# Performance work log

Hardware: AMD Instinct MI355X
Metric: run time of the kernel (lower is better)

The kernel has to match this reference:

```python
import jax, jax.numpy as jnp
import numpy as np

B, T, D, H, C = 8, 1024, 1024, 16, 8  # batch, seq, d_model, heads, num_concepts
DK = D // H
LAMBD = 5.0


def setup_inputs() -> dict:
    key = jax.random.key(0)
    ks = jax.random.split(key, 14)
    s = 0.02
    return {
        "qa_concept": jax.random.normal(ks[0], (B, T, T, C), jnp.float32),
        "query": jax.random.normal(ks[1], (B, T, D), jnp.float32),
        "key": jax.random.normal(ks[2], (B, T, D), jnp.float32),
        "value": jax.random.normal(ks[3], (B, T, D), jnp.float32),
        "Wq": jax.random.normal(ks[4], (D, D), jnp.float32) * s,
        "bq": jnp.zeros((D,), jnp.float32),
        "Wk": jax.random.normal(ks[5], (D, D), jnp.float32) * s,
        "bk": jnp.zeros((D,), jnp.float32),
        "Wv": jax.random.normal(ks[6], (D, D), jnp.float32) * s,
        "bv": jnp.zeros((D,), jnp.float32),
        "Wo": jax.random.normal(ks[7], (D, D), jnp.float32) * s,
        "bo": jnp.zeros((D,), jnp.float32),
        "mask": jax.random.randint(ks[8], (B, T), 0, 2, jnp.int32),
    }


def reference(qa_concept, query, key, value, Wq, bq, Wk, bk, Wv, bv, Wo, bo, mask):
    # Linear projections (torch Linear: y = x @ W.T + b)
    q = (query @ Wq.T + bq).reshape(B, T, H, DK).transpose(0, 2, 1, 3)  # [B,H,T,dk]
    k = (key @ Wk.T + bk).reshape(B, T, H, DK).transpose(0, 2, 1, 3)
    v = (value @ Wv.T + bv).reshape(B, T, H, DK).transpose(0, 2, 1, 3)
    scores = jnp.einsum("bhqd,bhkd->bhqk", q, k) / jnp.sqrt(jnp.float32(DK))
    # concept bias added to first C heads only
    bias = LAMBD * jnp.transpose(qa_concept, (0, 3, 1, 2))  # [B,C,T,T]
    scores = scores.at[:, :C, :, :].add(bias)
    # mask: [B,T] -> [B,1,1,T], fill -1e9 where 0
    scores = jnp.where(mask[:, None, None, :] == 0, jnp.float32(-1e9), scores)
    attn = jax.nn.softmax(scores, axis=-1)  # dropout is identity in eval
    x = jnp.einsum("bhqk,bhkd->bhqd", attn, v)
    x = x.transpose(0, 2, 1, 3).reshape(B, T, D)
    return x @ Wo.T + bo
```

## Files before the change

### kernel.cpp

```cpp
#include <hip/hip_runtime.h>

#define B_  8
#define T_  1024
#define D_  1024
#define H_  16
#define DK_ 64
#define C_  8
#define N_  (B_*T_)

typedef __attribute__((ext_vector_type(8))) short bf16x8;
typedef __attribute__((ext_vector_type(4))) float f32x4;
typedef __attribute__((ext_vector_type(8))) unsigned short u16x8;
typedef __attribute__((ext_vector_type(4))) unsigned short u16x4;

__device__ __forceinline__ float bf2f(unsigned short u) {
  union { unsigned int i; float f; } x; x.i = ((unsigned int)u) << 16; return x.f;
}
__device__ __forceinline__ unsigned short f2bf(float f) {
  union { float f; unsigned int i; } x; x.f = f;
  unsigned int r = (x.i + 0x7fffu + ((x.i >> 16) & 1u)) >> 16;
  return (unsigned short)r;
}
__device__ __forceinline__ unsigned short f2h(float f) {
  union { _Float16 h; unsigned short u; } x; x.h = (_Float16)f; return x.u;
}
__device__ __forceinline__ float h2f(unsigned short u) {
  union { _Float16 h; unsigned short u; } x; x.u = u; return (float)x.h;
}

__device__ __forceinline__ void gl_lds16(const unsigned short* g, unsigned short* l) {
  __builtin_amdgcn_global_load_lds(
      (const __attribute__((address_space(1))) unsigned int*)g,
      (__attribute__((address_space(3))) unsigned int*)l,
      16, 0, 0);
}

__global__ __launch_bounds__(256) void cvt_qkv(
    const float* __restrict__ q, const float* __restrict__ k,
    const float* __restrict__ v, unsigned short* __restrict__ qo,
    unsigned short* __restrict__ ko, unsigned short* __restrict__ vo, int n4) {
  int seg = blockIdx.x >> 10;
  int bid = blockIdx.x & 1023;
  const float* in = (seg == 0) ? q : (seg == 1) ? k : v;
  unsigned short* out = (seg == 0) ? qo : (seg == 1) ? ko : vo;
  int tid = bid * blockDim.x + threadIdx.x;
  int stride = 1024 * 256;
  const float4* in4 = (const float4*)in;
  u16x4* out4 = (u16x4*)out;
  for (int i = tid; i < n4; i += stride) {
    float4 vv = in4[i];
    u16x4 o = { f2bf(vv.x), f2bf(vv.y), f2bf(vv.z), f2bf(vv.w) };
    out4[i] = o;
  }
}

__global__ __launch_bounds__(256) void cvt_w(
    const float* __restrict__ w0, const float* __restrict__ w1,
    const float* __restrict__ w2, const float* __restrict__ w3,
    unsigned short* __restrict__ o0, unsigned short* __restrict__ o1,
    unsigned short* __restrict__ o2, unsigned short* __restrict__ o3, int n4) {
  int seg = blockIdx.x >> 8;
  int bid = blockIdx.x & 255;
  const float* in = (seg == 0) ? w0 : (seg == 1) ? w1 : (seg == 2) ? w2 : w3;
  unsigned short* out = (seg == 0) ? o0 : (seg == 1) ? o1 : (seg == 2) ? o2 : o3;
  int tid = bid * blockDim.x + threadIdx.x;
  int stride = 256 * 256;
  const float4* in4 = (const float4*)in;
  u16x4* out4 = (u16x4*)out;
  for (int i = tid; i < n4; i += stride) {
    float4 vv = in4[i];
    u16x4 o = { f2bf(vv.x), f2bf(vv.y), f2bf(vv.z), f2bf(vv.w) };
    out4[i] = o;
  }
}

__global__ __launch_bounds__(256) void transposeQa(
    const float* __restrict__ qa, unsigned short* __restrict__ qat) {
  int b = blockIdx.x >> 10, q = blockIdx.x & 1023;
  int t = threadIdx.x;
  __shared__ float L[8][132];
  const float* src = qa + ((size_t)(b*T_ + q))*T_*C_;
  for (int ch = 0; ch < 8; ++ch) {
    int k0 = ch*128;
    float4 v = *(const float4*)(src + (size_t)(k0 + (t>>1))*C_ + (t&1)*4);
    int c4 = (t&1)*4, kk = t>>1;
    L[c4+0][kk] = v.x; L[c4+1][kk] = v.y; L[c4+2][kk] = v.z; L[c4+3][kk] = v.w;
    __syncthreads();
    int c = t >> 5, kk2 = (t&31)*4;
    float4 p = *(const float4*)&L[c][kk2];
    u16x4 o = { f2h(p.x), f2h(p.y), f2h(p.z), f2h(p.w) };
    *(u16x4*)(qat + ((size_t)(b*C_ + c)*T_ + q)*T_ + k0 + kk2) = o;
    __syncthreads();
  }
}

__global__ __launch_bounds__(256) void transposeV(
    const unsigned short* __restrict__ V, unsigned short* __restrict__ Vt) {
  int bid = blockIdx.x;
  int tt = bid & 15;
  int bh = bid >> 4;
  int b = bh >> 4, h = bh & 15;
  __shared__ unsigned short L[64][72];
  int r  = threadIdx.x >> 3;
  int c8 = (threadIdx.x & 7) * 8;
  const unsigned short* src = V + ((size_t)(b*T_ + tt*64))*D_ + h*64;
#pragma unroll
  for (int p = 0; p < 2; ++p) {
    int rr = r + p*32;
    u16x8 v = *(const u16x8*)(src + (size_t)rr*D_ + c8);
    *(u16x8*)&L[rr][c8] = v;
  }
  __syncthreads();
  unsigned short* dst = Vt + ((size_t)bh*64)*T_ + tt*64;
#pragma unroll
  for (int p = 0; p < 2; ++p) {
    int d = r + p*32;
    u16x8 o;
#pragma unroll
    for (int i = 0; i < 8; ++i) o[i] = L[c8 + i][d];
    *(u16x8*)(dst + (size_t)d*T_ + c8) = o;
  }
}

template <bool OUT_F32>
__device__ __forceinline__ void gemm_body(
    int blockid, const unsigned short* __restrict__ X,
    const unsigned short* __restrict__ W, const float* __restrict__ bias,
    void* __restrict__ Yv, unsigned short* As, unsigned short* Bs) {
  int orig = (blockid & 7) * 64 + (blockid >> 3);
  int bm = orig >> 3, bn = orig & 7;
  int t = threadIdx.x, lane = t & 63, w = t >> 6;
  int wr = w >> 1, wc = w & 1;
  int r16 = lane & 15, kg = lane >> 4;

  int srow0 = lane >> 2;
  int scol  = (lane & 3) * 8;
  const unsigned short* Ab = X + (size_t)(bm*128)*D_ + scol;
  const unsigned short* Bb = W + (size_t)(bn*128)*D_ + scol;

  f32x4 acc[4][4];
#pragma unroll
  for (int m = 0; m < 4; ++m)
#pragma unroll
    for (int n = 0; n < 4; ++n) acc[m][n] = (f32x4){0.f,0.f,0.f,0.f};

  for (int k0 = 0; k0 < D_; k0 += 32) {
    __syncthreads();
#pragma unroll
    for (int c = 0; c < 2; ++c) {
      int cidx = w*2 + c;
      int row = cidx*16 + srow0;
      gl_lds16(Ab + (size_t)row*D_ + k0, As + cidx*512);
      gl_lds16(Bb + (size_t)row*D_ + k0, Bs + cidx*512);
    }
    __syncthreads();

    bf16x8 a[4], bb[4];
#pragma unroll
    for (int m = 0; m < 4; ++m)
      a[m] = *(const bf16x8*)(As + (wr*64 + m*16 + r16)*32 + kg*8);
#pragma unroll
    for (int n = 0; n < 4; ++n)
      bb[n] = *(const bf16x8*)(Bs + (wc*64 + n*16 + r16)*32 + kg*8);
#pragma unroll
    for (int m = 0; m < 4; ++m)
#pragma unroll
      for (int n = 0; n < 4; ++n)
        acc[m][n] = __builtin_amdgcn_mfma_f32_16x16x32_bf16(a[m], bb[n], acc[m][n], 0, 0, 0);
  }

#pragma unroll
  for (int n = 0; n < 4; ++n) {
    int col = bn*128 + wc*64 + n*16 + r16;
    float bv = bias[col];
#pragma unroll
    for (int m = 0; m < 4; ++m) {
      int row0 = bm*128 + wr*64 + m*16 + kg*4;
#pragma unroll
      for (int jj = 0; jj < 4; ++jj) {
        float rv = acc[m][n][jj] + bv;
        if constexpr (OUT_F32)
          ((float*)Yv)[(size_t)(row0 + jj)*D_ + col] = rv;
        else
          ((unsigned short*)Yv)[(size_t)(row0 + jj)*D_ + col] = f2bf(rv);
      }
    }
  }
}

template <bool OUT_F32>
__global__ __launch_bounds__(256) void gemm_lds(
    const unsigned short* __restrict__ X, const unsigned short* __restrict__ W,
    const float* __restrict__ bias, void* __restrict__ Yv) {
  __shared__ __align__(16) unsigned short As[128*32];
  __shared__ __align__(16) unsigned short Bs[128*32];
  gemm_body<OUT_F32>(blockIdx.x, X, W, bias, Yv, As, Bs);
}

__global__ __launch_bounds__(256) void gemm_qkv(
    const unsigned short* __restrict__ Xq, const unsigned short* __restrict__ Xk,
    const unsigned short* __restrict__ Xv,
    const unsigned short* __restrict__ Wq2, const unsigned short* __restrict__ Wk2,
    const unsigned short* __restrict__ Wv2,
    const float* __restrict__ bq2, const float* __restrict__ bk2,
    const float* __restrict__ bv2,
    unsigned short* __restrict__ Yq, unsigned short* __restrict__ Yk,
    unsigned short* __restrict__ Yv2) {
  __shared__ __align__(16) unsigned short As[128*32];
  __shared__ __align__(16) unsigned short Bs[128*32];
  int seg = blockIdx.x >> 9, inner = blockIdx.x & 511;
  const unsigned short* X = (seg == 0) ? Xq : (seg == 1) ? Xk : Xv;
  const unsigned short* W = (seg == 0) ? Wq2 : (seg == 1) ? Wk2 : Wv2;
  const float* bias = (seg == 0) ? bq2 : (seg == 1) ? bk2 : bv2;
  unsigned short* Y = (seg == 0) ? Yq : (seg == 1) ? Yk : Yv2;
  gemm_body<false>(inner, X, W, bias, Y, As, Bs);
}

__global__ __launch_bounds__(256, 3) void attn4b(
    const unsigned short* __restrict__ Q, const unsigned short* __restrict__ K,
    const unsigned short* __restrict__ Vt, const unsigned short* __restrict__ qat,
    const int* __restrict__ mask, unsigned short* __restrict__ X) {
  int swzid = ((blockIdx.x & 7) << 7) | (blockIdx.x >> 3);
  int qt = swzid & 7, h = (swzid >> 3) & 15, b = swzid >> 7;
  int w = threadIdx.x >> 6, lane = threadIdx.x & 63;
  int r16 = lane & 15, kg = lane >> 4;
  int q0w = qt*128 + w*32;
  int bh = b*H_ + h;

  __shared__ unsigned short Ks[2][64][64];
  __shared__ unsigned short Vs[2][64][64];
  __shared__ unsigned int  P32[4][2][16][32];

  int rl = lane >> 3;
  int eo = ((lane & 7) * 8) ^ (rl << 3);
  const unsigned short* Kb = K + ((size_t)b*T_)*D_ + h*DK_;
  const unsigned short* Vb = Vt + ((size_t)bh*DK_)*T_;

  int sw16 = (r16 & 7) << 4;
  int ko0 = ((kg*16 +  0) ^ sw16) >> 1;
  int ko1 = ((kg*16 + 64) ^ sw16) >> 1;
  int sw32 = (r16 & 7) << 2;

  bf16x8 qfr[2][2];
#pragma unroll
  for (int qf = 0; qf < 2; ++qf) {
    const unsigned short* qrow = Q + ((size_t)b*T_ + q0w + qf*16 + r16)*D_ + h*DK_ + kg*8;
    qfr[qf][0] = *(const bf16x8*)qrow;
    qfr[qf][1] = *(const bf16x8*)(qrow + 32);
  }

  f32x4 acc[2][4];
#pragma unroll
  for (int qf = 0; qf < 2; ++qf)
#pragma unroll
    for (int db = 0; db < 4; ++db) acc[qf][db] = (f32x4){0.f,0.f,0.f,0.f};
  float mold[2] = {-3e38f, -3e38f};
  float lpart[2] = {0.f, 0.f};

  const int* mrow = mask + b*T_;
  const unsigned short* qab0 = qat + ((size_t)((b*C_ + h)*T_) + q0w + r16)*T_;

#pragma unroll
  for (int c = 0; c < 2; ++c) {
    int cc = w*2 + c;
    gl_lds16(Kb + (size_t)(cc*8 + rl)*D_ + eo, &Ks[0][cc*8][0]);
    gl_lds16(Vb + (size_t)(cc*8 + rl)*T_ + eo, &Vs[0][cc*8][0]);
  }
  __syncthreads();

  for (int t = 0; t < 16; ++t) {
    int k0 = t*64, bb = t & 1;
    if (t < 15) {
      int kn = k0 + 64, nb = bb ^ 1;
#pragma unroll
      for (int c = 0; c < 2; ++c) {
        int cc = w*2 + c;
        gl_lds16(Kb + (size_t)(kn + cc*8 + rl)*D_ + eo, &Ks[nb][cc*8][0]);
        gl_lds16(Vb + (size_t)(cc*8 + rl)*T_ + kn + eo, &Vs[nb][cc*8][0]);
      }
    }
    u16x4 qv[2][4];
    if (h < C_) {
#pragma unroll
      for (int qf = 0; qf < 2; ++qf)
#pragma unroll
        for (int kt = 0; kt < 4; ++kt)
          qv[qf][kt] = *(const u16x4*)(qab0 + (size_t)qf*16*T_ + k0 + kt*16 + kg*4);
    }
    int mk = mrow[k0 + lane];
    unsigned long long bits = __ballot(mk != 0);

    f32x4 s[2][4];
#pragma unroll
    for (int kt = 0; kt < 4; ++kt) {
      bf16x8 kf0 = *(const bf16x8*)&Ks[bb][kt*16 + r16][ko0];
      bf16x8 kf1 = *(const bf16x8*)&Ks[bb][kt*16 + r16][ko1];
#pragma unroll
      for (int qf = 0; qf < 2; ++qf) {
        f32x4 z = (f32x4){0.f,0.f,0.f,0.f};
        z = __builtin_amdgcn_mfma_f32_16x16x32_bf16(kf0, qfr[qf][0], z, 0, 0, 0);
        z = __builtin_amdgcn_mfma_f32_16x16x32_bf16(kf1, qfr[qf][1], z, 0, 0, 0);
        s[qf][kt] = z;
      }
    }

    float pmaxq[2];
#pragma unroll
    for (int qf = 0; qf < 2; ++qf) {
      float pmax = -3e38f;
#pragma unroll
      for (int kt = 0; kt < 4; ++kt)
#pragma unroll
        for (int jj = 0; jj < 4; ++jj) {
          float v = s[qf][kt][jj] * 0.125f;
          if (h < C_) v += 5.0f * h2f(qv[qf][kt][jj]);
          int idx = kt*16 + kg*4 + jj;
          v = ((bits >> idx) & 1ULL) ? v : -1e9f;
          s[qf][kt][jj] = v;
          pmax = fmaxf(pmax, v);
        }
      pmax = fmaxf(pmax, __shfl_xor(pmax, 16, 64));
      pmax = fmaxf(pmax, __shfl_xor(pmax, 32, 64));
      pmaxq[qf] = pmax;
    }
    if (!__all(pmaxq[0] - mold[0] <= 8.0f && pmaxq[1] - mold[1] <= 8.0f)) {
#pragma unroll
      for (int qf = 0; qf < 2; ++qf) {
        float mnew = fmaxf(mold[qf], pmaxq[qf]);
        float sc = __expf(mold[qf] - mnew);
        mold[qf] = mnew;
        lpart[qf] *= sc;
        float scq[4];
#pragma unroll
        for (int jj = 0; jj < 4; ++jj) scq[jj] = __shfl(sc, kg*4 + jj, 64);
#pragma unroll
        for (int db = 0; db < 4; ++db)
#pragma unroll
          for (int jj = 0; jj < 4; ++jj) acc[qf][db][jj] *= scq[jj];
      }
    }
#pragma unroll
    for (int qf = 0; qf < 2; ++qf) {
      unsigned int pk[8];
#pragma unroll
      for (int kt = 0; kt < 4; ++kt) {
        float p0 = __expf(s[qf][kt][0] - mold[qf]), p1 = __expf(s[qf][kt][1] - mold[qf]);
        float p2 = __expf(s[qf][kt][2] - mold[qf]), p3 = __expf(s[qf][kt][3] - mold[qf]);
        lpart[qf] += (p0 + p1) + (p2 + p3);
        pk[kt*2+0] = (unsigned)f2bf(p0) | ((unsigned)f2bf(p1) << 16);
        pk[kt*2+1] = (unsigned)f2bf(p2) | ((unsigned)f2bf(p3) << 16);
      }
#pragma unroll
      for (int kt = 0; kt < 4; ++kt)
        *(uint2*)&P32[w][qf][r16][(kt*8 + kg*2) ^ sw32] =
            make_uint2(pk[kt*2], pk[kt*2+1]);
    }
    __builtin_amdgcn_sched_barrier(0);
    asm volatile("s_waitcnt lgkmcnt(0)");
    __builtin_amdgcn_sched_barrier(0);
#pragma unroll
    for (int qf = 0; qf < 2; ++qf) {
      bf16x8 pa0 = *(const bf16x8*)&P32[w][qf][r16][(kg*4) ^ sw32];
      bf16x8 pa1 = *(const bf16x8*)&P32[w][qf][r16][(16 + kg*4) ^ sw32];
#pragma unroll
      for (int db = 0; db < 4; ++db) {
        bf16x8 vf0 = *(const bf16x8*)&Vs[bb][db*16 + r16][ko0];
        bf16x8 vf1 = *(const bf16x8*)&Vs[bb][db*16 + r16][ko1];
        acc[qf][db] = __builtin_amdgcn_mfma_f32_16x16x32_bf16(pa0, vf0, acc[qf][db], 0, 0, 0);
        acc[qf][db] = __builtin_amdgcn_mfma_f32_16x16x32_bf16(pa1, vf1, acc[qf][db], 0, 0, 0);
      }
    }
    __syncthreads();
  }

#pragma unroll
  for (int qf = 0; qf < 2; ++qf) {
    float lp = lpart[qf];
    lp += __shfl_xor(lp, 16, 64);
    lp += __shfl_xor(lp, 32, 64);
    float linv = 1.0f / lp;
    float invq[4];
#pragma unroll
    for (int jj = 0; jj < 4; ++jj) invq[jj] = __shfl(linv, kg*4 + jj, 64);
#pragma unroll
    for (int jj = 0; jj < 4; ++jj)
#pragma unroll
      for (int db = 0; db < 4; ++db)
        X[((size_t)b*T_ + q0w + qf*16 + kg*4 + jj)*D_ + h*DK_ + db*16 + r16] =
            f2bf(acc[qf][db][jj] * invq[jj]);
  }
}

__global__ __launch_bounds__(256) void attn_fused(
    const unsigned short* __restrict__ Q, const unsigned short* __restrict__ K,
    const unsigned short* __restrict__ Vt, const float* __restrict__ qa,
    const int* __restrict__ mask, unsigned short* __restrict__ X) {
  int bid = blockIdx.x;
  int qt = bid & 15, h = (bid >> 4) & 15, b = bid >> 8;
  int w = threadIdx.x >> 6, lane = threadIdx.x & 63;
  int r16 = lane & 15, kg = lane >> 4;
  int q0 = qt*64 + w*16;
  int bh = b*H_ + h;

  __shared__ unsigned short P[4][16][72];

  const unsigned short* qrow = Q + ((size_t)b*T_ + q0 + r16)*D_ + h*DK_ + kg*8;
  bf16x8 qf0 = *(const bf16x8*)qrow;
  bf16x8 qf1 = *(const bf16x8*)(qrow + 32);

  f32x4 acc[4];
#pragma unroll
  for (int db = 0; db < 4; ++db) acc[db] = (f32x4){0.f,0.f,0.f,0.f};
  float mrow[4], lrow[4];
#pragma unroll
  for (int jj = 0; jj < 4; ++jj) { mrow[jj] = -3e38f; lrow[jj] = 0.f; }

  const int* mptr = mask + b*T_;
  const unsigned short* Kbase = K + ((size_t)b*T_)*D_ + h*DK_;
  const unsigned short* Vbase = Vt + ((size_t)bh*DK_)*T_;
  const float* qabase = qa + ((size_t)(b*T_ + q0 + kg*4))*T_*C_ + h;

  for (int k0 = 0; k0 < T_; k0 += 64) {
    f32x4 s[4];
#pragma unroll
    for (int kt = 0; kt < 4; ++kt) {
      const unsigned short* krow = Kbase + (size_t)(k0 + kt*16 + r16)*D_ + kg*8;
      f32x4 z = (f32x4){0.f,0.f,0.f,0.f};
      z = __builtin_amdgcn_mfma_f32_16x16x32_bf16(qf0, *(const bf16x8*)krow,        z, 0, 0, 0);
      z = __builtin_amdgcn_mfma_f32_16x16x32_bf16(qf1, *(const bf16x8*)(krow + 32), z, 0, 0, 0);
      s[kt] = z;
    }
    int mk[4];
#pragma unroll
    for (int kt = 0; kt < 4; ++kt) mk[kt] = mptr[k0 + kt*16 + r16];
    if (h < C_) {
#pragma unroll
      for (int kt = 0; kt < 4; ++kt)
#pragma unroll
        for (int jj = 0; jj < 4; ++jj) {
          float bb = qabase[(size_t)jj*T_*C_ + (size_t)(k0 + kt*16 + r16)*C_];
          s[kt][jj] = s[kt][jj]*0.125f + 5.0f*bb;
        }
    } else {
#pragma unroll
      for (int kt = 0; kt < 4; ++kt)
#pragma unroll
        for (int jj = 0; jj < 4; ++jj) s[kt][jj] *= 0.125f;
    }
#pragma unroll
    for (int kt = 0; kt < 4; ++kt)
#pragma unroll
      for (int jj = 0; jj < 4; ++jj)
        if (mk[kt] == 0) s[kt][jj] = -1e9f;

#pragma unroll
    for (int jj = 0; jj < 4; ++jj) {
      float v = fmaxf(fmaxf(s[0][jj], s[1][jj]), fmaxf(s[2][jj], s[3][jj]));
#pragma unroll
      for (int d = 1; d < 16; d <<= 1) v = fmaxf(v, __shfl_xor(v, d, 64));
      float mnew = fmaxf(mrow[jj], v);
      float sc = __expf(mrow[jj] - mnew);
      mrow[jj] = mnew;
      lrow[jj] *= sc;
#pragma unroll
      for (int db = 0; db < 4; ++db) acc[db][jj] *= sc;
      float rs = 0.f;
#pragma unroll
      for (int kt = 0; kt < 4; ++kt) {
        float p = __expf(s[kt][jj] - mnew);
        rs += p;
        P[w][kg*4 + jj][kt*16 + r16] = f2bf(p);
      }
#pragma unroll
      for (int d = 1; d < 16; d <<= 1) rs += __shfl_xor(rs, d, 64);
      lrow[jj] += rs;
    }
    __syncthreads();

    bf16x8 pa0 = *(const bf16x8*)&P[w][r16][kg*8];
    bf16x8 pa1 = *(const bf16x8*)&P[w][r16][32 + kg*8];
#pragma unroll
    for (int db = 0; db < 4; ++db) {
      const unsigned short* vr = Vbase + (size_t)(db*16 + r16)*T_ + k0 + kg*8;
      acc[db] = __builtin_amdgcn_mfma_f32_16x16x32_bf16(pa0, *(const bf16x8*)vr,        acc[db], 0, 0, 0);
      acc[db] = __builtin_amdgcn_mfma_f32_16x16x32_bf16(pa1, *(const bf16x8*)(vr + 32), acc[db], 0, 0, 0);
    }
  }

  float inv[4];
#pragma unroll
  for (int jj = 0; jj < 4; ++jj) inv[jj] = 1.0f / lrow[jj];
#pragma unroll
  for (int jj = 0; jj < 4; ++jj)
#pragma unroll
    for (int db = 0; db < 4; ++db)
      X[((size_t)b*T_ + q0 + kg*4 + jj)*D_ + h*DK_ + db*16 + r16] =
          f2bf(acc[db][jj] * inv[jj]);
}

extern "C" void kernel_launch(void* const* d_in, const int* in_sizes, int n_in,
                              void* d_out, int out_size, void* d_ws, size_t ws_size,
                              hipStream_t stream) {
  const float* qa    = (const float*)d_in[0];
  const float* query = (const float*)d_in[1];
  const float* key   = (const float*)d_in[2];
  const float* value = (const float*)d_in[3];
  const float* Wq = (const float*)d_in[4];
  const float* bq = (const float*)d_in[5];
  const float* Wk = (const float*)d_in[6];
  const float* bk = (const float*)d_in[7];
  const float* Wv = (const float*)d_in[8];
  const float* bv = (const float*)d_in[9];
  const float* Wo = (const float*)d_in[10];
  const float* bo = (const float*)d_in[11];
  const int* mask = (const int*)d_in[12];

  const size_t ND = (size_t)N_ * D_;
  const size_t DD = (size_t)D_ * D_;
  const size_t QAT = (size_t)B_ * C_ * T_ * T_;
  unsigned short* Qws = (unsigned short*)d_ws;
  unsigned short* Kws = Qws + ND;
  unsigned short* Vws = Kws + ND;
  unsigned short* Xws = Vws + ND;
  unsigned short* qbf = Xws + ND;
  unsigned short* kbf = qbf + ND;
  unsigned short* vbf = kbf + ND;
  unsigned short* wqbf = vbf + ND;
  unsigned short* wkbf = wqbf + DD;
  unsigned short* wvbf = wkbf + DD;
  unsigned short* wobf = wvbf + DD;
  unsigned short* qatws = wobf + DD;
  unsigned short* Vtws = qbf;

  bool fast = ws_size >= (7*ND + 4*DD + QAT) * sizeof(unsigned short);

  dim3 blk(256);
  cvt_qkv<<<3072, blk, 0, stream>>>(query, key, value, qbf, kbf, vbf, (int)(ND/4));
  cvt_w<<<1024, blk, 0, stream>>>(Wq, Wk, Wv, Wo, wqbf, wkbf, wvbf, wobf, (int)(DD/4));

  gemm_qkv<<<3*512, blk, 0, stream>>>(qbf, kbf, vbf, wqbf, wkbf, wvbf,
                                      bq, bk, bv, Qws, Kws, Vws);

  transposeV<<<B_*H_*(T_/64), blk, 0, stream>>>(Vws, Vtws);

  if (fast) {
    transposeQa<<<B_*T_, blk, 0, stream>>>(qa, qatws);
    attn4b<<<B_*H_*(T_/128), blk, 0, stream>>>(Qws, Kws, Vtws, qatws, mask, Xws);
  } else {
    attn_fused<<<B_*H_*(T_/64), blk, 0, stream>>>(Qws, Kws, Vtws, qa, mask, Xws);
  }

  gemm_lds<true><<<512, blk, 0, stream>>>(Xws, wobf, bo, (float*)d_out);
}
```

Baseline: 324.2 us.

## Merge conversion kernels, deepen GEMM K-tile, and hoist V fragment loads

Three unrelated changes. The two fp32-to-bf16 conversion kernels become one launch, removing a kernel boundary. The shared GEMM body now stages 64-wide K tiles (doubling LDS per block) so there are half as many barrier pairs per K sweep. In the attention kernel the V fragments are loaded from LDS before the softmax instead of inside the PV MFMA loop, overlapping LDS latency with softmax math at the cost of more registers, which matters under the 3-blocks-per-CU bound.

```diff
diff --git a/kernel.cpp b/kernel.cpp
--- a/kernel.cpp
+++ b/kernel.cpp
@@ -35,36 +35,34 @@
       16, 0, 0);
 }
 
-__global__ __launch_bounds__(256) void cvt_qkv(
+__global__ __launch_bounds__(256) void cvt_all(
     const float* __restrict__ q, const float* __restrict__ k,
-    const float* __restrict__ v, unsigned short* __restrict__ qo,
-    unsigned short* __restrict__ ko, unsigned short* __restrict__ vo, int n4) {
-  int seg = blockIdx.x >> 10;
-  int bid = blockIdx.x & 1023;
-  const float* in = (seg == 0) ? q : (seg == 1) ? k : v;
-  unsigned short* out = (seg == 0) ? qo : (seg == 1) ? ko : vo;
-  int tid = bid * blockDim.x + threadIdx.x;
-  int stride = 1024 * 256;
-  const float4* in4 = (const float4*)in;
-  u16x4* out4 = (u16x4*)out;
-  for (int i = tid; i < n4; i += stride) {
-    float4 vv = in4[i];
-    u16x4 o = { f2bf(vv.x), f2bf(vv.y), f2bf(vv.z), f2bf(vv.w) };
-    out4[i] = o;
-  }
-}
-
-__global__ __launch_bounds__(256) void cvt_w(
+    const float* __restrict__ v,
     const float* __restrict__ w0, const float* __restrict__ w1,
     const float* __restrict__ w2, const float* __restrict__ w3,
+    unsigned short* __restrict__ qo, unsigned short* __restrict__ ko,
+    unsigned short* __restrict__ vo,
     unsigned short* __restrict__ o0, unsigned short* __restrict__ o1,
-    unsigned short* __restrict__ o2, unsigned short* __restrict__ o3, int n4) {
-  int seg = blockIdx.x >> 8;
-  int bid = blockIdx.x & 255;
-  const float* in = (seg == 0) ? w0 : (seg == 1) ? w1 : (seg == 2) ? w2 : w3;
-  unsigned short* out = (seg == 0) ? o0 : (seg == 1) ? o1 : (seg == 2) ? o2 : o3;
-  int tid = bid * blockDim.x + threadIdx.x;
-  int stride = 256 * 256;
+    unsigned short* __restrict__ o2, unsigned short* __restrict__ o3,
+    int n4q, int n4w) {
+  int seg = blockIdx.x >> 10;
+  const float* in;
+  unsigned short* out;
+  int tid, stride, n4;
+  if (seg < 3) {
+    in  = (seg == 0) ? q : (seg == 1) ? k : v;
+    out = (seg == 0) ? qo : (seg == 1) ? ko : vo;
+    tid = (blockIdx.x & 1023) * 256 + threadIdx.x;
+    stride = 1024 * 256;
+    n4 = n4q;
+  } else {
+    int sub = (blockIdx.x & 1023) >> 8;
+    in  = (sub == 0) ? w0 : (sub == 1) ? w1 : (sub == 2) ? w2 : w3;
+    out = (sub == 0) ? o0 : (sub == 1) ? o1 : (sub == 2) ? o2 : o3;
+    tid = (blockIdx.x & 255) * 256 + threadIdx.x;
+    stride = 256 * 256;
+    n4 = n4w;
+  }
   const float4* in4 = (const float4*)in;
   u16x4* out4 = (u16x4*)out;
   for (int i = tid; i < n4; i += stride) {
@@ -133,8 +131,8 @@
   int wr = w >> 1, wc = w & 1;
   int r16 = lane & 15, kg = lane >> 4;
 
-  int srow0 = lane >> 2;
-  int scol  = (lane & 3) * 8;
+  int srow0 = lane >> 3;
+  int scol  = (lane & 7) * 8;
   const unsigned short* Ab = X + (size_t)(bm*128)*D_ + scol;
   const unsigned short* Bb = W + (size_t)(bn*128)*D_ + scol;
 
@@ -144,29 +142,32 @@
 #pragma unroll
     for (int n = 0; n < 4; ++n) acc[m][n] = (f32x4){0.f,0.f,0.f,0.f};
 
-  for (int k0 = 0; k0 < D_; k0 += 32) {
+  for (int k0 = 0; k0 < D_; k0 += 64) {
     __syncthreads();
 #pragma unroll
-    for (int c = 0; c < 2; ++c) {
-      int cidx = w*2 + c;
-      int row = cidx*16 + srow0;
+    for (int c = 0; c < 4; ++c) {
+      int cidx = w*4 + c;
+      int row = cidx*8 + srow0;
       gl_lds16(Ab + (size_t)row*D_ + k0, As + cidx*512);
       gl_lds16(Bb + (size_t)row*D_ + k0, Bs + cidx*512);
     }
     __syncthreads();
 
-    bf16x8 a[4], bb[4];
-#pragma unroll
-    for (int m = 0; m < 4; ++m)
-      a[m] = *(const bf16x8*)(As + (wr*64 + m*16 + r16)*32 + kg*8);
-#pragma unroll
-    for (int n = 0; n < 4; ++n)
-      bb[n] = *(const bf16x8*)(Bs + (wc*64 + n*16 + r16)*32 + kg*8);
-#pragma unroll
-    for (int m = 0; m < 4; ++m)
+#pragma unroll
+    for (int kk = 0; kk < 64; kk += 32) {
+      bf16x8 a[4], bb[4];
+#pragma unroll
+      for (int m = 0; m < 4; ++m)
+        a[m] = *(const bf16x8*)(As + (wr*64 + m*16 + r16)*64 + kk + kg*8);
 #pragma unroll
       for (int n = 0; n < 4; ++n)
-        acc[m][n] = __builtin_amdgcn_mfma_f32_16x16x32_bf16(a[m], bb[n], acc[m][n], 0, 0, 0);
+        bb[n] = *(const bf16x8*)(Bs + (wc*64 + n*16 + r16)*64 + kk + kg*8);
+#pragma unroll
+      for (int m = 0; m < 4; ++m)
+#pragma unroll
+        for (int n = 0; n < 4; ++n)
+          acc[m][n] = __builtin_amdgcn_mfma_f32_16x16x32_bf16(a[m], bb[n], acc[m][n], 0, 0, 0);
+    }
   }
 
 #pragma unroll
@@ -192,8 +193,8 @@
 __global__ __launch_bounds__(256) void gemm_lds(
     const unsigned short* __restrict__ X, const unsigned short* __restrict__ W,
     const float* __restrict__ bias, void* __restrict__ Yv) {
-  __shared__ __align__(16) unsigned short As[128*32];
-  __shared__ __align__(16) unsigned short Bs[128*32];
+  __shared__ __align__(16) unsigned short As[128*64];
+  __shared__ __align__(16) unsigned short Bs[128*64];
   gemm_body<OUT_F32>(blockIdx.x, X, W, bias, Yv, As, Bs);
 }
 
@@ -206,8 +207,8 @@
     const float* __restrict__ bv2,
     unsigned short* __restrict__ Yq, unsigned short* __restrict__ Yk,
     unsigned short* __restrict__ Yv2) {
-  __shared__ __align__(16) unsigned short As[128*32];
-  __shared__ __align__(16) unsigned short Bs[128*32];
+  __shared__ __align__(16) unsigned short As[128*64];
+  __shared__ __align__(16) unsigned short Bs[128*64];
   int seg = blockIdx.x >> 9, inner = blockIdx.x & 511;
   const unsigned short* X = (seg == 0) ? Xq : (seg == 1) ? Xk : Xv;
   const unsigned short* W = (seg == 0) ? Wq2 : (seg == 1) ? Wk2 : Wv2;
@@ -216,7 +217,7 @@
   gemm_body<false>(inner, X, W, bias, Y, As, Bs);
 }
 
-__global__ __launch_bounds__(256, 3) void attn4b(
+__global__ __launch_bounds__(256, 3) void attn4d(
     const unsigned short* __restrict__ Q, const unsigned short* __restrict__ K,
     const unsigned short* __restrict__ Vt, const unsigned short* __restrict__ qat,
     const int* __restrict__ mask, unsigned short* __restrict__ X) {
@@ -302,6 +303,12 @@
         z = __builtin_amdgcn_mfma_f32_16x16x32_bf16(kf1, qfr[qf][1], z, 0, 0, 0);
         s[qf][kt] = z;
       }
+    }
+    bf16x8 vf[4][2];
+#pragma unroll
+    for (int db = 0; db < 4; ++db) {
+      vf[db][0] = *(const bf16x8*)&Vs[bb][db*16 + r16][ko0];
+      vf[db][1] = *(const bf16x8*)&Vs[bb][db*16 + r16][ko1];
     }
 
     float pmaxq[2];
@@ -364,10 +371,8 @@
       bf16x8 pa1 = *(const bf16x8*)&P32[w][qf][r16][(16 + kg*4) ^ sw32];
 #pragma unroll
       for (int db = 0; db < 4; ++db) {
-        bf16x8 vf0 = *(const bf16x8*)&Vs[bb][db*16 + r16][ko0];
-        bf16x8 vf1 = *(const bf16x8*)&Vs[bb][db*16 + r16][ko1];
-        acc[qf][db] = __builtin_amdgcn_mfma_f32_16x16x32_bf16(pa0, vf0, acc[qf][db], 0, 0, 0);
-        acc[qf][db] = __builtin_amdgcn_mfma_f32_16x16x32_bf16(pa1, vf1, acc[qf][db], 0, 0, 0);
+        acc[qf][db] = __builtin_amdgcn_mfma_f32_16x16x32_bf16(pa0, vf[db][0], acc[qf][db], 0, 0, 0);
+        acc[qf][db] = __builtin_amdgcn_mfma_f32_16x16x32_bf16(pa1, vf[db][1], acc[qf][db], 0, 0, 0);
       }
     }
     __syncthreads();
@@ -535,8 +540,9 @@
   bool fast = ws_size >= (7*ND + 4*DD + QAT) * sizeof(unsigned short);
 
   dim3 blk(256);
-  cvt_qkv<<<3072, blk, 0, stream>>>(query, key, value, qbf, kbf, vbf, (int)(ND/4));
-  cvt_w<<<1024, blk, 0, stream>>>(Wq, Wk, Wv, Wo, wqbf, wkbf, wvbf, wobf, (int)(DD/4));
+  cvt_all<<<4096, blk, 0, stream>>>(query, key, value, Wq, Wk, Wv, Wo,
+                                    qbf, kbf, vbf, wqbf, wkbf, wvbf, wobf,
+                                    (int)(ND/4), (int)(DD/4));
 
   gemm_qkv<<<3*512, blk, 0, stream>>>(qbf, kbf, vbf, wqbf, wkbf, wvbf,
                                       bq, bk, bv, Qws, Kws, Vws);
@@ -545,7 +551,7 @@
 
   if (fast) {
     transposeQa<<<B_*T_, blk, 0, stream>>>(qa, qatws);
-    attn4b<<<B_*H_*(T_/128), blk, 0, stream>>>(Qws, Kws, Vtws, qatws, mask, Xws);
+    attn4d<<<B_*H_*(T_/128), blk, 0, stream>>>(Qws, Kws, Vtws, qatws, mask, Xws);
   } else {
     attn_fused<<<B_*H_*(T_/64), blk, 0, stream>>>(Qws, Kws, Vtws, qa, mask, Xws);
   }
```

Result: slower. 470.7 us (+45.2%).
